# Kernel optimization log

Hardware: AMD Instinct MI355X
Metric: run time of the kernel (lower is better)

## Reference

```python
import jax, jax.numpy as jnp
import numpy as np
import math

B, S, D, H = 4, 1024, 1024, 16
Dh = D // H
THETA = 10000.0
LAMBDA_INIT = 0.8  # current_lambda_init_for_scaling (no set_lambda_init_for_scaling call)
GN_EPS = 1e-5


def setup_inputs() -> dict:
    key = jax.random.key(0)
    ks = jax.random.split(key, 14)
    w = 0.02
    return {
        "x_norm": jax.random.normal(ks[0], (B, S, D), jnp.float32),
        "learned_lambda": jax.random.uniform(ks[1], (), jnp.float32),
        "hierarchical_mask_C": jax.random.uniform(ks[2], (1, 1, S, S), jnp.float32),
        "padding_mask": jnp.ones((B, S), jnp.int32),
        "wq_w": jax.random.normal(ks[3], (2 * D, D), jnp.float32) * w,
        "wq_b": jnp.zeros((2 * D,), jnp.float32),
        "wk_w": jax.random.normal(ks[4], (2 * D, D), jnp.float32) * w,
        "wk_b": jnp.zeros((2 * D,), jnp.float32),
        "wv_w": jax.random.normal(ks[5], (D, D), jnp.float32) * w,
        "wv_b": jnp.zeros((D,), jnp.float32),
        "out_w": jax.random.normal(ks[6], (D, D), jnp.float32) * w,
        "out_b": jnp.zeros((D,), jnp.float32),
        "gn_w": jnp.ones((D,), jnp.float32),
        "gn_b": jnp.zeros((D,), jnp.float32),
    }


def _rope_tables(seq_len):
    freqs = 1.0 / (THETA ** (jnp.arange(0, Dh, 2, dtype=jnp.float32) / Dh))  # [Dh/2]
    t = jnp.arange(seq_len, dtype=jnp.float32)
    ang = jnp.outer(t, freqs)  # [S, Dh/2]
    return jnp.cos(ang), jnp.sin(ang)


def _apply_rope(x, cos, sin):
    # x: [B,H,S,Dh]; cos/sin: [S,Dh/2] broadcast over B,H
    x1, x2 = x[..., : Dh // 2], x[..., Dh // 2 :]
    return jnp.concatenate((x1 * cos - x2 * sin, x1 * sin + x2 * cos), axis=-1)


def _heads(x):
    # [B,S,D] -> [B,H,S,Dh]
    b, s, _ = x.shape
    return x.reshape(b, s, H, Dh).transpose(0, 2, 1, 3)


def _masked_softmax(q, k, key_pad_bad):
    scores = jnp.einsum("bhqd,bhkd->bhqk", q, k) / math.sqrt(Dh)
    scores = jnp.where(key_pad_bad[:, None, None, :], -1e9, scores)
    return jax.nn.softmax(scores, axis=-1)


def reference(x_norm, learned_lambda, hierarchical_mask_C, padding_mask,
              wq_w, wq_b, wk_w, wk_b, wv_w, wv_b, out_w, out_b, gn_w, gn_b):
    b, s, _ = x_norm.shape
    q_proj = x_norm @ wq_w.T + wq_b  # [B,S,2D]
    k_proj = x_norm @ wk_w.T + wk_b
    v_proj = x_norm @ wv_w.T + wv_b
    q1, q2 = _heads(q_proj[..., :D]), _heads(q_proj[..., D:])
    k1, k2 = _heads(k_proj[..., :D]), _heads(k_proj[..., D:])
    v = _heads(v_proj)

    cos, sin = _rope_tables(s)
    q1, k1 = _apply_rope(q1, cos, sin), _apply_rope(k1, cos, sin)
    q2, k2 = _apply_rope(q2, cos, sin), _apply_rope(k2, cos, sin)

    key_pad_bad = padding_mask == 0  # [B,S]
    a1 = _masked_softmax(q1, k1, key_pad_bad)
    a2 = _masked_softmax(q2, k2, key_pad_bad)
    diff = a1 - learned_lambda * a2
    combined = hierarchical_mask_C * diff  # [B,H,S,S]

    ctx = jnp.einsum("bhqk,bhkd->bhqd", combined, v)  # [B,H,S,Dh]
    merged = ctx.transpose(0, 2, 1, 3).reshape(b, s, D)  # [B,S,D]

    # GroupNorm(n_heads, d_model) applied on [B, D, S]: normalize per (batch, head-group)
    g = merged.reshape(b, s, H, Dh)
    mean = g.mean(axis=(1, 3), keepdims=True)
    var = ((g - mean) ** 2).mean(axis=(1, 3), keepdims=True)
    normed = ((g - mean) * jax.lax.rsqrt(var + GN_EPS)).reshape(b, s, D)
    normed = normed * gn_w + gn_b

    scaled = normed * (1.0 - LAMBDA_INIT)
    output = scaled @ out_w.T + out_b
    return output, a1, a2
```

## Files before the change

### kernel.cpp

```cpp
#include <hip/hip_runtime.h>
#include <hip/hip_bf16.h>
#include <hip/hip_fp16.h>
#include <cstdint>

#define HSZ    4194304ull
#define S_LEN  1024
#define NHEAD  16
#define DH     64

typedef __attribute__((ext_vector_type(8))) short bf16x8;
typedef __attribute__((ext_vector_type(8))) unsigned short u16x8;
typedef __attribute__((ext_vector_type(4))) unsigned short u16x4;
typedef __attribute__((ext_vector_type(4))) float f32x4;
#define MFMA(a,b,c) __builtin_amdgcn_mfma_f32_16x16x32_bf16(a,b,c,0,0,0)

__device__ __forceinline__ unsigned short f2bf(float f) {
    union { float f; uint32_t u; } v; v.f = f;
    uint32_t r = (v.u + 0x7fffu + ((v.u >> 16) & 1u)) >> 16;
    return (unsigned short)r;
}
__device__ __forceinline__ float bf2f(unsigned short u) {
    union { uint32_t u; float f; } v; v.u = (uint32_t)u << 16;
    return v.f;
}
__device__ __forceinline__ unsigned short f2h(float f) { return __half_as_ushort(__float2half(f)); }
__device__ __forceinline__ float h2f(unsigned short u) { return __half2float(__ushort_as_half(u)); }

__device__ __forceinline__ void bar_lds() {
    asm volatile("s_waitcnt lgkmcnt(0)" ::: "memory");
    __builtin_amdgcn_s_barrier();
}

__global__ __launch_bounds__(256) void conv_x_kernel(
    const float* __restrict__ X, unsigned short* __restrict__ xh, unsigned short* __restrict__ xl)
{
    const int idx = blockIdx.x * 256 + threadIdx.x;
    float4 a = *(const float4*)&X[idx * 8];
    float4 b = *(const float4*)&X[idx * 8 + 4];
    float v[8] = {a.x, a.y, a.z, a.w, b.x, b.y, b.z, b.w};
    u16x8 hi, lo;
#pragma unroll
    for (int j = 0; j < 8; ++j) {
        unsigned short h = f2bf(v[j]);
        hi[j] = h;
        lo[j] = f2bf(v[j] - bf2f(h));
    }
    *(u16x8*)&xh[idx * 8] = hi;
    *(u16x8*)&xl[idx * 8] = lo;
}

__global__ __launch_bounds__(256) void conv_w_kernel(
    const float* __restrict__ wq, const float* __restrict__ wk,
    const float* __restrict__ wv, const float* __restrict__ wo,
    unsigned short* __restrict__ Wcat)
{
    const int idx = blockIdx.x * 256 + threadIdx.x;
    const int row = idx >> 7;
    const int cg  = idx & 127;
    const float* src;
    int rl;
    if (row < 2048)      { src = wq; rl = row; }
    else if (row < 4096) { src = wk; rl = row - 2048; }
    else if (row < 5120) { src = wv; rl = row - 4096; }
    else                 { src = wo; rl = row - 5120; }
    float4 a = *(const float4*)&src[(size_t)rl * 1024 + cg * 8];
    float4 b = *(const float4*)&src[(size_t)rl * 1024 + cg * 8 + 4];
    float v[8] = {a.x, a.y, a.z, a.w, b.x, b.y, b.z, b.w};
    u16x8 o;
#pragma unroll
    for (int j = 0; j < 8; ++j) o[j] = f2bf(v[j]);
    *(u16x8*)&Wcat[(size_t)row * 1024 + cg * 8] = o;
}

__global__ __launch_bounds__(256) void conv_c_kernel(
    const float* __restrict__ C, unsigned short* __restrict__ Cb)
{
    const int idx = blockIdx.x * 256 + threadIdx.x;
    float4 a = *(const float4*)&C[idx * 8];
    float4 b = *(const float4*)&C[idx * 8 + 4];
    float v[8] = {a.x, a.y, a.z, a.w, b.x, b.y, b.z, b.w};
    u16x8 o;
#pragma unroll
    for (int j = 0; j < 8; ++j) o[j] = f2bf(v[j]);
    *(u16x8*)&Cb[idx * 8] = o;
}

__global__ __launch_bounds__(256) void proj_mfma_kernel(
    const unsigned short* __restrict__ xh, const unsigned short* __restrict__ xl,
    const unsigned short* __restrict__ Wcat,
    const float* __restrict__ bq, const float* __restrict__ bk, const float* __restrict__ bv,
    unsigned short* __restrict__ qk, unsigned short* __restrict__ vt)
{
    __shared__ __align__(16) unsigned short Ah[128 * 64];
    __shared__ __align__(16) unsigned short Al[128 * 64];
    __shared__ __align__(16) unsigned short Bs[128 * 64];

    const int t   = threadIdx.x;
    const int bid = blockIdx.x;
    const int swz = (bid & 7) * 160 + (bid >> 3);
    const int n_idx = swz % 40, m_idx = swz / 40;
    const int m0 = m_idx * 128, n0 = n_idx * 128;
    const int w = t >> 6, l = t & 63, ln = l & 15, kg = l >> 4;
    const int wm = w >> 1, wn = w & 1;
    const bool useLo = (n0 < 2048);

    f32x4 acc[4][4];
#pragma unroll
    for (int i = 0; i < 4; ++i)
#pragma unroll
        for (int j = 0; j < 4; ++j) acc[i][j] = (f32x4){0.f, 0.f, 0.f, 0.f};

    for (int k0 = 0; k0 < 1024; k0 += 64) {
        __syncthreads();
#pragma unroll
        for (int i = 0; i < 4; ++i) {
            const int e   = t + i * 256;
            const int row = e >> 3, cg = e & 7;
            const int off = (row * 128 + cg * 16) ^ ((row & 7) << 4);
            const size_t ga = (size_t)(m0 + row) * 1024 + k0 + cg * 8;
            const size_t gb = (size_t)(n0 + row) * 1024 + k0 + cg * 8;
            *(bf16x8*)((char*)Ah + off) = *(const bf16x8*)(xh + ga);
            if (useLo)
                *(bf16x8*)((char*)Al + off) = *(const bf16x8*)(xl + ga);
            *(bf16x8*)((char*)Bs + off) = *(const bf16x8*)(Wcat + gb);
        }
        __syncthreads();
#pragma unroll
        for (int ks = 0; ks < 2; ++ks) {
            bf16x8 bfrag[4];
#pragma unroll
            for (int nj = 0; nj < 4; ++nj) {
                const int row = wn * 64 + nj * 16 + ln;
                const int off = (row * 128 + ks * 64 + kg * 16) ^ ((row & 7) << 4);
                bfrag[nj] = *(const bf16x8*)((const char*)Bs + off);
            }
#pragma unroll
            for (int mi = 0; mi < 4; ++mi) {
                const int row = wm * 64 + mi * 16 + ln;
                const int off = (row * 128 + ks * 64 + kg * 16) ^ ((row & 7) << 4);
                bf16x8 ah = *(const bf16x8*)((const char*)Ah + off);
#pragma unroll
                for (int nj = 0; nj < 4; ++nj)
                    acc[mi][nj] = MFMA(ah, bfrag[nj], acc[mi][nj]);
                if (useLo) {
                    bf16x8 al = *(const bf16x8*)((const char*)Al + off);
#pragma unroll
                    for (int nj = 0; nj < 4; ++nj)
                        acc[mi][nj] = MFMA(al, bfrag[nj], acc[mi][nj]);
                }
            }
        }
    }

    const int seg = (n0 < 2048) ? 0 : (n0 < 4096 ? 1 : 2);
    if (seg < 2) {
        const float* bias = (seg == 0) ? bq : bk;
#pragma unroll
        for (int njp = 0; njp < 2; ++njp) {
            const int n1  = n0 + wn * 64 + njp * 16 + ln;
            const int nl1 = n1 - seg * 2048;
            const int head = (nl1 >> 6) & 15;
            const int dd   = nl1 & 63;
            const float bb1 = bias[nl1];
            const float bb2 = bias[nl1 + 32];
            const float freq = exp2f((float)dd * (-13.287712379549449f / 32.0f));
            unsigned short* hiT;
            unsigned short* loT = nullptr;
            if (seg == 0) {
                const int tq = (nl1 >> 10);
                hiT = qk + (size_t)(tq * 2)     * HSZ;
                loT = qk + (size_t)(tq * 2 + 1) * HSZ;
            } else {
                hiT = qk + (size_t)(4 + (nl1 >> 10)) * HSZ;
            }
#pragma unroll
            for (int mi = 0; mi < 4; ++mi) {
                const int mb = m0 + wm * 64 + mi * 16 + kg * 4;
#pragma unroll
                for (int r = 0; r < 4; ++r) {
                    const int m = mb + r, b_ = m >> 10, s = m & 1023;
                    float sn, cs;
                    sincosf((float)s * freq, &sn, &cs);
                    const float x1 = acc[mi][njp][r]     + bb1;
                    const float x2 = acc[mi][njp + 2][r] + bb2;
                    const float r1 = x1 * cs - x2 * sn;
                    const float r2 = x1 * sn + x2 * cs;
                    const size_t base = (((size_t)(b_ * 16 + head)) * 1024 + s) * 64;
                    const unsigned short h1 = f2bf(r1), h2 = f2bf(r2);
                    hiT[base + dd]      = h1;
                    hiT[base + dd + 32] = h2;
                    if (seg == 0) {
                        loT[base + dd]      = f2bf(r1 - bf2f(h1));
                        loT[base + dd + 32] = f2bf(r2 - bf2f(h2));
                    }
                }
            }
        }
    } else {
#pragma unroll
        for (int mi = 0; mi < 4; ++mi) {
#pragma unroll
            for (int nj = 0; nj < 4; ++nj) {
                const int n  = n0 + wn * 64 + nj * 16 + ln;
                const int nl = n - 4096;
                const float bb = bv[nl];
                const int head = nl >> 6, d = nl & 63;
                const int mb = m0 + wm * 64 + mi * 16 + kg * 4;
                const int b = mb >> 10, sb = mb & 1023;
                u16x4 o;
#pragma unroll
                for (int r = 0; r < 4; ++r) o[r] = f2bf(acc[mi][nj][r] + bb);
                *(u16x4*)(vt + ((size_t)(b * 16 + head) * 64 + d) * 1024 + sb) = o;
            }
        }
    }
}

__global__ __launch_bounds__(512, 4) void attn_kernel(
    const unsigned short* __restrict__ qk,
    const unsigned short* __restrict__ vt,
    const unsigned short* __restrict__ Cb,
    const int* __restrict__ pad,
    const float* __restrict__ lam_p,
    float* __restrict__ out_a1, float* __restrict__ out_a2,
    float* __restrict__ merged)
{
    __shared__ __align__(16) unsigned short sc1[16][1032];
    __shared__ __align__(16) unsigned short sc2[16][1032];
    __shared__ __align__(16) float pmax1[16][8];
    __shared__ __align__(16) float pmax2[16][8];
    __shared__ __align__(16) f32x4 red[256];

    const int t  = threadIdx.x;
    const int w  = t >> 6;
    const int l  = t & 63;
    const int ln = l & 15;
    const int g  = l >> 4;
    const int kf = g * 8;

    const int flat = blockIdx.x;
    const int virt = (flat & 7) * 512 + (flat >> 3);
    const int bh = virt >> 6, b = bh >> 4, h = bh & 15;
    const int q0 = (virt & 63) * 16;
    const float lam = lam_p[0];

    const f32x4 Z = {0.f, 0.f, 0.f, 0.f};
    f32x4 ctx = Z;
    const int dt  = w & 3;
    const int khf = w >> 2;

    uint32_t padm = 0;
#pragma unroll
    for (int j = 0; j < 8; ++j)
        padm |= (pad[b * S_LEN + w * 128 + j * 16 + ln] != 0 ? 1u : 0u) << j;

    const unsigned short* Q1h = qk + (size_t)0 * HSZ + (size_t)bh * 65536;
    const unsigned short* Q1l = qk + (size_t)1 * HSZ + (size_t)bh * 65536;
    const unsigned short* Q2h = qk + (size_t)2 * HSZ + (size_t)bh * 65536;
    const unsigned short* Q2l = qk + (size_t)3 * HSZ + (size_t)bh * 65536;
    const unsigned short* K1  = qk + (size_t)4 * HSZ + (size_t)bh * 65536;
    const unsigned short* K2  = qk + (size_t)5 * HSZ + (size_t)bh * 65536;

    const size_t qb = (size_t)(q0 + ln) * 64 + kf;
    const bf16x8 q1h0 = *(const bf16x8*)(Q1h + qb);
    const bf16x8 q1h1 = *(const bf16x8*)(Q1h + qb + 32);
    const bf16x8 q1l0 = *(const bf16x8*)(Q1l + qb);
    const bf16x8 q1l1 = *(const bf16x8*)(Q1l + qb + 32);
    const bf16x8 q2h0 = *(const bf16x8*)(Q2h + qb);
    const bf16x8 q2h1 = *(const bf16x8*)(Q2h + qb + 32);
    const bf16x8 q2l0 = *(const bf16x8*)(Q2l + qb);
    const bf16x8 q2l1 = *(const bf16x8*)(Q2l + qb + 32);

    {
        f32x4 m1 = {-3.4e38f, -3.4e38f, -3.4e38f, -3.4e38f};
#pragma unroll 2
        for (int j = 0; j < 8; ++j) {
            const int key = w * 128 + j * 16 + ln;
            const size_t kb = (size_t)key * 64 + kf;
            const bf16x8 k0 = *(const bf16x8*)(K1 + kb);
            const bf16x8 k1 = *(const bf16x8*)(K1 + kb + 32);
            f32x4 a = Z;
            a = MFMA(q1h0, k0, a); a = MFMA(q1h1, k1, a);
            a = MFMA(q1l0, k0, a); a = MFMA(q1l1, k1, a);
            const bool ok = (padm >> j) & 1;
            const float mm = ok ? 0.125f : 0.0f;
            const float ma = ok ? 0.0f : -60000.0f;
#pragma unroll
            for (int r = 0; r < 4; ++r) {
                const float sv = a[r] * mm + ma;
                m1[r] = fmaxf(m1[r], sv);
                sc1[g * 4 + r][key] = f2h(sv);
            }
        }
#pragma unroll
        for (int off = 1; off < 16; off <<= 1)
#pragma unroll
            for (int r = 0; r < 4; ++r) m1[r] = fmaxf(m1[r], __shfl_xor(m1[r], off));
        if (ln == 0) {
#pragma unroll
            for (int r = 0; r < 4; ++r) pmax1[g * 4 + r][w] = m1[r];
        }
        f32x4 m2 = {-3.4e38f, -3.4e38f, -3.4e38f, -3.4e38f};
#pragma unroll 2
        for (int j = 0; j < 8; ++j) {
            const int key = w * 128 + j * 16 + ln;
            const size_t kb = (size_t)key * 64 + kf;
            const bf16x8 k0 = *(const bf16x8*)(K2 + kb);
            const bf16x8 k1 = *(const bf16x8*)(K2 + kb + 32);
            f32x4 a = Z;
            a = MFMA(q2h0, k0, a); a = MFMA(q2h1, k1, a);
            a = MFMA(q2l0, k0, a); a = MFMA(q2l1, k1, a);
            const bool ok = (padm >> j) & 1;
            const float mm = ok ? 0.125f : 0.0f;
            const float ma = ok ? 0.0f : -60000.0f;
#pragma unroll
            for (int r = 0; r < 4; ++r) {
                const float sv = a[r] * mm + ma;
                m2[r] = fmaxf(m2[r], sv);
                sc2[g * 4 + r][key] = f2h(sv);
            }
        }
#pragma unroll
        for (int off = 1; off < 16; off <<= 1)
#pragma unroll
            for (int r = 0; r < 4; ++r) m2[r] = fmaxf(m2[r], __shfl_xor(m2[r], off));
        if (ln == 0) {
#pragma unroll
            for (int r = 0; r < 4; ++r) pmax2[g * 4 + r][w] = m2[r];
        }
    }
    bar_lds();

    {
        const int row = t >> 5, ci = t & 31;
        float fm1 = -3.4e38f, fm2 = -3.4e38f;
#pragma unroll
        for (int wi = 0; wi < 8; ++wi) {
            fm1 = fmaxf(fm1, pmax1[row][wi]);
            fm2 = fmaxf(fm2, pmax2[row][wi]);
        }
        float sum1 = 0.f, sum2 = 0.f;
#pragma unroll 2
        for (int it = 0; it < 4; ++it) {
            const int c0 = ci * 8 + it * 256;
            const u16x8 xv1 = *(const u16x8*)&sc1[row][c0];
            const u16x8 xv2 = *(const u16x8*)&sc2[row][c0];
            u16x8 ev1, ev2;
#pragma unroll
            for (int i = 0; i < 8; ++i) {
                const float e1 = __expf(h2f(xv1[i]) - fm1);
                const float e2 = __expf(h2f(xv2[i]) - fm2);
                sum1 += e1; sum2 += e2;
                ev1[i] = f2h(e1); ev2[i] = f2h(e2);
            }
            *(u16x8*)&sc1[row][c0] = ev1;
            *(u16x8*)&sc2[row][c0] = ev2;
        }
#pragma unroll
        for (int off = 1; off < 32; off <<= 1) {
            sum1 += __shfl_xor(sum1, off);
            sum2 += __shfl_xor(sum2, off);
        }
        const float inv1 = 1.0f / sum1;
        const float inv2 = 1.0f / sum2;
        float* aout1 = out_a1 + ((size_t)bh * S_LEN + q0 + row) * S_LEN;
        float* aout2 = out_a2 + ((size_t)bh * S_LEN + q0 + row) * S_LEN;
        const unsigned short* Crow = Cb + (size_t)(q0 + row) * S_LEN;
#pragma unroll 2
        for (int it = 0; it < 4; ++it) {
            const int c0 = ci * 8 + it * 256;
            const u16x8 ev1 = *(const u16x8*)&sc1[row][c0];
            const u16x8 ev2 = *(const u16x8*)&sc2[row][c0];
            const u16x8 cv  = *(const u16x8*)&Crow[c0];
            float av1[8], av2[8];
#pragma unroll
            for (int i = 0; i < 8; ++i) {
                av1[i] = h2f(ev1[i]) * inv1;
                av2[i] = h2f(ev2[i]) * inv2;
            }
            f32x4 oa1 = {av1[0], av1[1], av1[2], av1[3]};
            f32x4 ob1 = {av1[4], av1[5], av1[6], av1[7]};
            f32x4 oa2 = {av2[0], av2[1], av2[2], av2[3]};
            f32x4 ob2 = {av2[4], av2[5], av2[6], av2[7]};
            __builtin_nontemporal_store(oa1, (f32x4*)&aout1[c0]);
            __builtin_nontemporal_store(ob1, (f32x4*)&aout1[c0 + 4]);
            __builtin_nontemporal_store(oa2, (f32x4*)&aout2[c0]);
            __builtin_nontemporal_store(ob2, (f32x4*)&aout2[c0 + 4]);
            u16x8 cw;
#pragma unroll
            for (int i = 0; i < 8; ++i)
                cw[i] = f2bf(bf2f(cv[i]) * (av1[i] - lam * av2[i]));
            *(u16x8*)&sc1[row][c0] = cw;
        }
    }
    bar_lds();

    {
        const unsigned short* vtb = vt + (size_t)bh * 65536
                                       + (size_t)(dt * 16 + ln) * S_LEN + kf;
#pragma unroll 4
        for (int ks = 0; ks < 16; ++ks) {
            const int kk = khf * 16 + ks;
            const bf16x8 A0 = *(const bf16x8*)&sc1[ln][kk * 32 + kf];
            const bf16x8 Bv = *(const bf16x8*)(vtb + kk * 32);
            ctx = MFMA(A0, Bv, ctx);
        }
    }

    __syncthreads();
    if (khf == 1) red[dt * 64 + l] = ctx;
    __syncthreads();
    if (khf == 0) {
        ctx += red[dt * 64 + l];
        const int col = h * DH + dt * 16 + ln;
#pragma unroll
        for (int r = 0; r < 4; ++r)
            merged[(size_t)(b * S_LEN + q0 + g * 4 + r) * 1024 + col] = ctx[r];
    }
}

__global__ __launch_bounds__(256) void stats_kernel(
    const float* __restrict__ merged, float* __restrict__ stats)
{
    const int g = blockIdx.x;
    const int b = g >> 4, h = g & 15;
    const int t = threadIdx.x;
    float sum = 0.f, sq = 0.f;
    for (int i = t; i < 65536; i += 256) {
        const int s = i >> 6, d = i & 63;
        const float v = merged[((size_t)(b * S_LEN + s)) * 1024 + h * DH + d];
        sum += v; sq += v * v;
    }
#pragma unroll
    for (int off = 32; off > 0; off >>= 1) {
        sum += __shfl_xor(sum, off);
        sq  += __shfl_xor(sq, off);
    }
    __shared__ float rs[4], rq[4];
    const int wid = t >> 6;
    if ((t & 63) == 0) { rs[wid] = sum; rq[wid] = sq; }
    __syncthreads();
    if (t == 0) {
        const float S = rs[0] + rs[1] + rs[2] + rs[3];
        const float Q = rq[0] + rq[1] + rq[2] + rq[3];
        const float mean = S * (1.0f / 65536.0f);
        const float var  = Q * (1.0f / 65536.0f) - mean * mean;
        stats[2*g]   = mean;
        stats[2*g+1] = rsqrtf(var + 1e-5f);
    }
}

__global__ __launch_bounds__(256) void norm_conv_kernel(
    const float* __restrict__ merged, const float* __restrict__ stats,
    const float* __restrict__ gw, const float* __restrict__ gb,
    unsigned short* __restrict__ normed)
{
    const int idx = blockIdx.x * 256 + threadIdx.x;
    const int m = idx >> 7;
    const int col8 = (idx & 127) * 8;
    const int b = m >> 10, h = col8 >> 6;
    const float mean = stats[2 * (b * 16 + h)];
    const float inv  = stats[2 * (b * 16 + h) + 1];
    float4 v0 = *(const float4*)&merged[(size_t)m * 1024 + col8];
    float4 v1 = *(const float4*)&merged[(size_t)m * 1024 + col8 + 4];
    float4 w0 = *(const float4*)&gw[col8];
    float4 w1 = *(const float4*)&gw[col8 + 4];
    float4 g0 = *(const float4*)&gb[col8];
    float4 g1 = *(const float4*)&gb[col8 + 4];
    float v[8] = {v0.x, v0.y, v0.z, v0.w, v1.x, v1.y, v1.z, v1.w};
    float wv[8] = {w0.x, w0.y, w0.z, w0.w, w1.x, w1.y, w1.z, w1.w};
    float gv[8] = {g0.x, g0.y, g0.z, g0.w, g1.x, g1.y, g1.z, g1.w};
    u16x8 o;
#pragma unroll
    for (int j = 0; j < 8; ++j)
        o[j] = f2bf(((v[j] - mean) * inv * wv[j] + gv[j]) * 0.2f);
    *(u16x8*)&normed[(size_t)m * 1024 + col8] = o;
}

__global__ __launch_bounds__(256) void out_mfma_kernel(
    const unsigned short* __restrict__ An, const unsigned short* __restrict__ Wo_bf,
    const float* __restrict__ bo, float* __restrict__ out)
{
    __shared__ __align__(16) unsigned short As[128 * 64];
    __shared__ __align__(16) unsigned short Bs[128 * 64];

    const int t   = threadIdx.x;
    const int bid = blockIdx.x;
    const int swz = (bid & 7) * 32 + (bid >> 3);
    const int n_idx = swz & 7, m_idx = swz >> 3;
    const int m0 = m_idx * 128, n0 = n_idx * 128;
    const int w = t >> 6, l = t & 63, ln = l & 15, kg = l >> 4;
    const int wm = w >> 1, wn = w & 1;

    f32x4 acc[4][4];
#pragma unroll
    for (int i = 0; i < 4; ++i)
#pragma unroll
        for (int j = 0; j < 4; ++j) acc[i][j] = (f32x4){0.f, 0.f, 0.f, 0.f};

    for (int k0 = 0; k0 < 1024; k0 += 64) {
        __syncthreads();
#pragma unroll
        for (int i = 0; i < 4; ++i) {
            const int e   = t + i * 256;
            const int row = e >> 3, cg = e & 7;
            const int off = (row * 128 + cg * 16) ^ ((row & 7) << 4);
            *(bf16x8*)((char*)As + off) = *(const bf16x8*)(An + (size_t)(m0 + row) * 1024 + k0 + cg * 8);
            *(bf16x8*)((char*)Bs + off) = *(const bf16x8*)(Wo_bf + (size_t)(n0 + row) * 1024 + k0 + cg * 8);
        }
        __syncthreads();
#pragma unroll
        for (int ks = 0; ks < 2; ++ks) {
            bf16x8 bfrag[4];
#pragma unroll
            for (int nj = 0; nj < 4; ++nj) {
                const int row = wn * 64 + nj * 16 + ln;
                const int off = (row * 128 + ks * 64 + kg * 16) ^ ((row & 7) << 4);
                bfrag[nj] = *(const bf16x8*)((const char*)Bs + off);
            }
#pragma unroll
            for (int mi = 0; mi < 4; ++mi) {
                const int row = wm * 64 + mi * 16 + ln;
                const int off = (row * 128 + ks * 64 + kg * 16) ^ ((row & 7) << 4);
                bf16x8 af = *(const bf16x8*)((const char*)As + off);
#pragma unroll
                for (int nj = 0; nj < 4; ++nj)
                    acc[mi][nj] = MFMA(af, bfrag[nj], acc[mi][nj]);
            }
        }
    }

#pragma unroll
    for (int mi = 0; mi < 4; ++mi) {
#pragma unroll
        for (int nj = 0; nj < 4; ++nj) {
            const int n = n0 + wn * 64 + nj * 16 + ln;
            const float bb = bo[n];
            const int mb = m0 + wm * 64 + mi * 16 + kg * 4;
#pragma unroll
            for (int r = 0; r < 4; ++r)
                out[(size_t)(mb + r) * 1024 + n] = acc[mi][nj][r] + bb;
        }
    }
}

extern "C" void kernel_launch(void* const* d_in, const int* in_sizes, int n_in,
                              void* d_out, int out_size, void* d_ws, size_t ws_size,
                              hipStream_t stream)
{
    const float* x   = (const float*)d_in[0];
    const float* lam = (const float*)d_in[1];
    const float* C   = (const float*)d_in[2];
    const int*   pad = (const int*)  d_in[3];
    const float* wq  = (const float*)d_in[4];
    const float* bq  = (const float*)d_in[5];
    const float* wk  = (const float*)d_in[6];
    const float* bk  = (const float*)d_in[7];
    const float* wv  = (const float*)d_in[8];
    const float* bv  = (const float*)d_in[9];
    const float* wo  = (const float*)d_in[10];
    const float* bo  = (const float*)d_in[11];
    const float* gw  = (const float*)d_in[12];
    const float* gb  = (const float*)d_in[13];

    float* out = (float*)d_out;
    float* a1  = out + 4194304;
    float* a2  = a1 + 67108864;

    unsigned short* xh   = (unsigned short*)d_ws;
    unsigned short* xl   = xh + HSZ;
    unsigned short* qk   = xl + HSZ;
    unsigned short* vt   = qk + 6 * HSZ;
    unsigned short* Wcat = vt + HSZ;
    float* merged        = (float*)(Wcat + 6144ull * 1024);
    float* stats         = merged + HSZ;
    unsigned short* normed = (unsigned short*)(stats + 128);
    unsigned short* Cb   = xh;

    conv_x_kernel<<<2048, 256, 0, stream>>>(x, xh, xl);
    conv_w_kernel<<<3072, 256, 0, stream>>>(wq, wk, wv, wo, Wcat);
    proj_mfma_kernel<<<1280, 256, 0, stream>>>(xh, xl, Wcat, bq, bk, bv, qk, vt);
    conv_c_kernel<<<512, 256, 0, stream>>>(C, Cb);
    attn_kernel<<<4096, 512, 0, stream>>>(qk, vt, Cb, pad, lam, a1, a2, merged);
    stats_kernel<<<64, 256, 0, stream>>>(merged, stats);
    norm_conv_kernel<<<2048, 256, 0, stream>>>(merged, stats, gw, gb, normed);
    out_mfma_kernel<<<256, 256, 0, stream>>>(normed, Wcat + 5120ull * 1024, bo, out);
}
```

Baseline: 527.9 us.

## Swizzle attention score LDS, unroll QK loops, fuse groupnorm into output GEMM

```diff
diff --git a/kernel.cpp b/kernel.cpp
--- a/kernel.cpp
+++ b/kernel.cpp
@@ -29,6 +29,15 @@
 __device__ __forceinline__ void bar_lds() {
     asm volatile("s_waitcnt lgkmcnt(0)" ::: "memory");
     __builtin_amdgcn_s_barrier();
+}
+
+__device__ __forceinline__ unsigned short* scp(unsigned short* base, int row, int col) {
+    const int byte = (col * 2) ^ ((row & 7) << 4);
+    return (unsigned short*)((char*)(base + row * 1032) + byte);
+}
+__device__ __forceinline__ const unsigned short* scp(const unsigned short* base, int row, int col) {
+    const int byte = (col * 2) ^ ((row & 7) << 4);
+    return (const unsigned short*)((const char*)(base + row * 1032) + byte);
 }
 
 __global__ __launch_bounds__(256) void conv_x_kernel(
@@ -225,8 +234,8 @@
     float* __restrict__ out_a1, float* __restrict__ out_a2,
     float* __restrict__ merged)
 {
-    __shared__ __align__(16) unsigned short sc1[16][1032];
-    __shared__ __align__(16) unsigned short sc2[16][1032];
+    __shared__ __align__(16) unsigned short sc1[16 * 1032];
+    __shared__ __align__(16) unsigned short sc2[16 * 1032];
     __shared__ __align__(16) float pmax1[16][8];
     __shared__ __align__(16) float pmax2[16][8];
     __shared__ __align__(16) f32x4 red[256];
@@ -273,7 +282,7 @@
 
     {
         f32x4 m1 = {-3.4e38f, -3.4e38f, -3.4e38f, -3.4e38f};
-#pragma unroll 2
+#pragma unroll 4
         for (int j = 0; j < 8; ++j) {
             const int key = w * 128 + j * 16 + ln;
             const size_t kb = (size_t)key * 64 + kf;
@@ -289,7 +298,7 @@
             for (int r = 0; r < 4; ++r) {
                 const float sv = a[r] * mm + ma;
                 m1[r] = fmaxf(m1[r], sv);
-                sc1[g * 4 + r][key] = f2h(sv);
+                *scp(sc1, g * 4 + r, key) = f2h(sv);
             }
         }
 #pragma unroll
@@ -301,7 +310,7 @@
             for (int r = 0; r < 4; ++r) pmax1[g * 4 + r][w] = m1[r];
         }
         f32x4 m2 = {-3.4e38f, -3.4e38f, -3.4e38f, -3.4e38f};
-#pragma unroll 2
+#pragma unroll 4
         for (int j = 0; j < 8; ++j) {
             const int key = w * 128 + j * 16 + ln;
             const size_t kb = (size_t)key * 64 + kf;
@@ -317,7 +326,7 @@
             for (int r = 0; r < 4; ++r) {
                 const float sv = a[r] * mm + ma;
                 m2[r] = fmaxf(m2[r], sv);
-                sc2[g * 4 + r][key] = f2h(sv);
+                *scp(sc2, g * 4 + r, key) = f2h(sv);
             }
         }
 #pragma unroll
@@ -343,8 +352,8 @@
 #pragma unroll 2
         for (int it = 0; it < 4; ++it) {
             const int c0 = ci * 8 + it * 256;
-            const u16x8 xv1 = *(const u16x8*)&sc1[row][c0];
-            const u16x8 xv2 = *(const u16x8*)&sc2[row][c0];
+            const u16x8 xv1 = *(const u16x8*)scp(sc1, row, c0);
+            const u16x8 xv2 = *(const u16x8*)scp(sc2, row, c0);
             u16x8 ev1, ev2;
 #pragma unroll
             for (int i = 0; i < 8; ++i) {
@@ -353,8 +362,8 @@
                 sum1 += e1; sum2 += e2;
                 ev1[i] = f2h(e1); ev2[i] = f2h(e2);
             }
-            *(u16x8*)&sc1[row][c0] = ev1;
-            *(u16x8*)&sc2[row][c0] = ev2;
+            *(u16x8*)scp(sc1, row, c0) = ev1;
+            *(u16x8*)scp(sc2, row, c0) = ev2;
         }
 #pragma unroll
         for (int off = 1; off < 32; off <<= 1) {
@@ -369,8 +378,8 @@
 #pragma unroll 2
         for (int it = 0; it < 4; ++it) {
             const int c0 = ci * 8 + it * 256;
-            const u16x8 ev1 = *(const u16x8*)&sc1[row][c0];
-            const u16x8 ev2 = *(const u16x8*)&sc2[row][c0];
+            const u16x8 ev1 = *(const u16x8*)scp(sc1, row, c0);
+            const u16x8 ev2 = *(const u16x8*)scp(sc2, row, c0);
             const u16x8 cv  = *(const u16x8*)&Crow[c0];
             float av1[8], av2[8];
 #pragma unroll
@@ -390,7 +399,7 @@
 #pragma unroll
             for (int i = 0; i < 8; ++i)
                 cw[i] = f2bf(bf2f(cv[i]) * (av1[i] - lam * av2[i]));
-            *(u16x8*)&sc1[row][c0] = cw;
+            *(u16x8*)scp(sc1, row, c0) = cw;
         }
     }
     bar_lds();
@@ -401,7 +410,7 @@
 #pragma unroll 4
         for (int ks = 0; ks < 16; ++ks) {
             const int kk = khf * 16 + ks;
-            const bf16x8 A0 = *(const bf16x8*)&sc1[ln][kk * 32 + kf];
+            const bf16x8 A0 = *(const bf16x8*)scp(sc1, ln, kk * 32 + kf);
             const bf16x8 Bv = *(const bf16x8*)(vtb + kk * 32);
             ctx = MFMA(A0, Bv, ctx);
         }
@@ -450,35 +459,10 @@
     }
 }
 
-__global__ __launch_bounds__(256) void norm_conv_kernel(
+__global__ __launch_bounds__(256) void out_mfma_kernel(
     const float* __restrict__ merged, const float* __restrict__ stats,
     const float* __restrict__ gw, const float* __restrict__ gb,
-    unsigned short* __restrict__ normed)
-{
-    const int idx = blockIdx.x * 256 + threadIdx.x;
-    const int m = idx >> 7;
-    const int col8 = (idx & 127) * 8;
-    const int b = m >> 10, h = col8 >> 6;
-    const float mean = stats[2 * (b * 16 + h)];
-    const float inv  = stats[2 * (b * 16 + h) + 1];
-    float4 v0 = *(const float4*)&merged[(size_t)m * 1024 + col8];
-    float4 v1 = *(const float4*)&merged[(size_t)m * 1024 + col8 + 4];
-    float4 w0 = *(const float4*)&gw[col8];
-    float4 w1 = *(const float4*)&gw[col8 + 4];
-    float4 g0 = *(const float4*)&gb[col8];
-    float4 g1 = *(const float4*)&gb[col8 + 4];
-    float v[8] = {v0.x, v0.y, v0.z, v0.w, v1.x, v1.y, v1.z, v1.w};
-    float wv[8] = {w0.x, w0.y, w0.z, w0.w, w1.x, w1.y, w1.z, w1.w};
-    float gv[8] = {g0.x, g0.y, g0.z, g0.w, g1.x, g1.y, g1.z, g1.w};
-    u16x8 o;
-#pragma unroll
-    for (int j = 0; j < 8; ++j)
-        o[j] = f2bf(((v[j] - mean) * inv * wv[j] + gv[j]) * 0.2f);
-    *(u16x8*)&normed[(size_t)m * 1024 + col8] = o;
-}
-
-__global__ __launch_bounds__(256) void out_mfma_kernel(
-    const unsigned short* __restrict__ An, const unsigned short* __restrict__ Wo_bf,
+    const unsigned short* __restrict__ Wo_bf,
     const float* __restrict__ bo, float* __restrict__ out)
 {
     __shared__ __align__(16) unsigned short As[128 * 64];
@@ -505,8 +489,29 @@
             const int e   = t + i * 256;
             const int row = e >> 3, cg = e & 7;
             const int off = (row * 128 + cg * 16) ^ ((row & 7) << 4);
-            *(bf16x8*)((char*)As + off) = *(const bf16x8*)(An + (size_t)(m0 + row) * 1024 + k0 + cg * 8);
-            *(bf16x8*)((char*)Bs + off) = *(const bf16x8*)(Wo_bf + (size_t)(n0 + row) * 1024 + k0 + cg * 8);
+            const int col8 = k0 + cg * 8;
+            {
+                const int m  = m0 + row;
+                const int bb = m >> 10;
+                const int hh = col8 >> 6;
+                const float mean = stats[2 * (bb * 16 + hh)];
+                const float inv  = stats[2 * (bb * 16 + hh) + 1];
+                float4 v0 = *(const float4*)&merged[(size_t)m * 1024 + col8];
+                float4 v1 = *(const float4*)&merged[(size_t)m * 1024 + col8 + 4];
+                float4 w0 = *(const float4*)&gw[col8];
+                float4 w1 = *(const float4*)&gw[col8 + 4];
+                float4 g0 = *(const float4*)&gb[col8];
+                float4 g1 = *(const float4*)&gb[col8 + 4];
+                float v[8]  = {v0.x, v0.y, v0.z, v0.w, v1.x, v1.y, v1.z, v1.w};
+                float wv[8] = {w0.x, w0.y, w0.z, w0.w, w1.x, w1.y, w1.z, w1.w};
+                float gv[8] = {g0.x, g0.y, g0.z, g0.w, g1.x, g1.y, g1.z, g1.w};
+                u16x8 o;
+#pragma unroll
+                for (int j = 0; j < 8; ++j)
+                    o[j] = f2bf(((v[j] - mean) * inv * wv[j] + gv[j]) * 0.2f);
+                *(u16x8*)((char*)As + off) = o;
+            }
+            *(bf16x8*)((char*)Bs + off) = *(const bf16x8*)(Wo_bf + (size_t)(n0 + row) * 1024 + col8);
         }
         __syncthreads();
 #pragma unroll
@@ -574,7 +579,6 @@
     unsigned short* Wcat = vt + HSZ;
     float* merged        = (float*)(Wcat + 6144ull * 1024);
     float* stats         = merged + HSZ;
-    unsigned short* normed = (unsigned short*)(stats + 128);
     unsigned short* Cb   = xh;
 
     conv_x_kernel<<<2048, 256, 0, stream>>>(x, xh, xl);
@@ -583,6 +587,5 @@
     conv_c_kernel<<<512, 256, 0, stream>>>(C, Cb);
     attn_kernel<<<4096, 512, 0, stream>>>(qk, vt, Cb, pad, lam, a1, a2, merged);
     stats_kernel<<<64, 256, 0, stream>>>(merged, stats);
-    norm_conv_kernel<<<2048, 256, 0, stream>>>(merged, stats, gw, gb, normed);
-    out_mfma_kernel<<<256, 256, 0, stream>>>(normed, Wcat + 5120ull * 1024, bo, out);
-}
+    out_mfma_kernel<<<256, 256, 0, stream>>>(merged, stats, gw, gb, Wcat + 5120ull * 1024, bo, out);
+}
```

After: 539.7 us. 1.02x slower.
